# Kernel tuning notes

Measured on AMD Instinct MI355X. Metric: run time of the kernel, lower is better.

Reference implementation:

```python
import jax, jax.numpy as jnp
import numpy as np

NUM_HEADS = 16
ROPE_BASE = 10000.0


def _rope_cos_sin(T, head_dim, dtype):
    # standard rotary: angles[t, i] = t * base^(-2i/head_dim), half-split layout
    inv_freq = 1.0 / (ROPE_BASE ** (jnp.arange(0, head_dim, 2, dtype=jnp.float32) / head_dim))
    ang = jnp.arange(T, dtype=jnp.float32)[:, None] * inv_freq[None, :]  # [T, hd/2]
    cos = jnp.concatenate([jnp.cos(ang), jnp.cos(ang)], axis=-1).astype(dtype)  # [T, hd]
    sin = jnp.concatenate([jnp.sin(ang), jnp.sin(ang)], axis=-1).astype(dtype)
    return cos, sin


def _rotate_half(t):
    t1, t2 = jnp.split(t, 2, axis=-1)
    return jnp.concatenate([-t2, t1], axis=-1)


def _apply_rope(t, cos, sin):
    # t: [B, H, T, hd]; cos/sin: [T, hd]
    return t * cos[None, None] + _rotate_half(t) * sin[None, None]


def setup_inputs() -> dict:
    key = jax.random.key(0)
    B, T, C = 2, 2048, 1024
    k1, k2, k3 = jax.random.split(key, 3)
    x = jax.random.normal(k1, (B, T, C), dtype=jnp.float32)
    w_attn = jax.random.normal(k2, (C, 3 * C), dtype=jnp.float32) * (C ** -0.5)
    w_proj = jax.random.normal(k3, (C, C), dtype=jnp.float32) * (C ** -0.5)
    return {"x": x, "w_attn": w_attn, "w_proj": w_proj}


def reference(x, w_attn, w_proj):
    B, T, C = x.shape
    H = NUM_HEADS
    hd = C // H

    qkv = x @ w_attn  # [B, T, 3C]
    q, k, v = jnp.split(qkv, 3, axis=-1)
    # [B, T, C] -> [B, H, T, hd]
    q = q.reshape(B, T, H, hd).transpose(0, 2, 1, 3)
    k = k.reshape(B, T, H, hd).transpose(0, 2, 1, 3)
    v = v.reshape(B, T, H, hd).transpose(0, 2, 1, 3)

    cos, sin = _rope_cos_sin(T, hd, x.dtype)
    q = _apply_rope(q, cos, sin)
    k = _apply_rope(k, cos, sin)

    scale = 1.0 / np.sqrt(hd).astype(np.float32)
    att = jnp.einsum('bhqd,bhkd->bhqk', q, k) * scale  # [B, H, T, T]
    causal = jnp.tril(jnp.ones((T, T), dtype=bool))
    att = jnp.where(causal[None, None], att, jnp.array(-jnp.inf, dtype=att.dtype))
    att = jax.nn.softmax(att, axis=-1)
    y = jnp.einsum('bhqk,bhkd->bhqd', att, v)  # [B, H, T, hd]
    y = y.transpose(0, 2, 1, 3).reshape(B, T, C)
    return y @ w_proj
```

## Files before the change

### kernel.cpp

```cpp
#include <hip/hip_runtime.h>

typedef unsigned short u16;
typedef unsigned int u32;
typedef unsigned long long u64;
typedef __attribute__((ext_vector_type(8))) short s16x8;
typedef __attribute__((ext_vector_type(8))) __bf16 bf16x8;
typedef __attribute__((ext_vector_type(4))) float fx4;
typedef __attribute__((ext_vector_type(16))) float fx16;
typedef __attribute__((ext_vector_type(2))) u32 u32x2;
typedef __attribute__((ext_vector_type(4))) u32 u32x4;

__device__ __forceinline__ fx4 mfma_16x16x32(s16x8 a, s16x8 b, fx4 c) {
  return __builtin_amdgcn_mfma_f32_16x16x32_bf16(
      __builtin_bit_cast(bf16x8, a), __builtin_bit_cast(bf16x8, b), c, 0, 0, 0);
}
__device__ __forceinline__ fx16 mfma_32x32x16(s16x8 a, s16x8 b, fx16 c) {
  return __builtin_amdgcn_mfma_f32_32x32x16_bf16(
      __builtin_bit_cast(bf16x8, a), __builtin_bit_cast(bf16x8, b), c, 0, 0, 0);
}

__device__ __forceinline__ u16 f2bf(float f) {
  u32 u = __builtin_bit_cast(u32, f);
  u32 r = u + 0x7fffu + ((u >> 16) & 1u);
  return (u16)(r >> 16);
}
__device__ __forceinline__ float bf2f(u16 h) {
  u32 u = ((u32)h) << 16;
  return __builtin_bit_cast(float, u);
}

__device__ __forceinline__ u32 cvtpk(float lo, float hi) {
  u32 r;
  asm("v_cvt_pk_bf16_f32 %0, %1, %2" : "=v"(r) : "v"(lo), "v"(hi));
  return r;
}

__device__ __forceinline__ float max3f(float a, float b, float c) {
  float r;
  asm("v_max3_f32 %0, %1, %2, %3" : "=v"(r) : "v"(a), "v"(b), "v"(c));
  return r;
}

__device__ __forceinline__ void plswap(u32& x, u32& y) {
  typedef __attribute__((ext_vector_type(2))) unsigned int uix2;
  uix2 r = __builtin_amdgcn_permlane32_swap(x, y, false, false);
  x = r[0];
  y = r[1];
}

__device__ __forceinline__ float xhalf_max(float v) {
  u32 a = __builtin_bit_cast(u32, v), b = a;
  plswap(a, b);
  return fmaxf(__builtin_bit_cast(float, a), __builtin_bit_cast(float, b));
}
__device__ __forceinline__ float xhalf_sum(float v) {
  u32 a = __builtin_bit_cast(u32, v), b = a;
  plswap(a, b);
  return __builtin_bit_cast(float, a) + __builtin_bit_cast(float, b);
}

__device__ __forceinline__ void gload16(const void* g, void* l) {
  __builtin_amdgcn_global_load_lds(
      (const __attribute__((address_space(1))) u32*)g,
      (__attribute__((address_space(3))) u32*)l, 16, 0, 0);
}

#define B_ 2
#define T_ 2048
#define C_ 1024
#define H_ 16
#define HD_ 64
#define BH_ 32
#define M_ 4096
#define CF_ 0.18033688011112042f

__global__ __launch_bounds__(256) void prep_k(
    const float* __restrict__ x, const float* __restrict__ wa,
    const float* __restrict__ wp, u16* __restrict__ xb, u16* __restrict__ waT,
    u16* __restrict__ wpT, float* __restrict__ ct, float* __restrict__ st) {
  __shared__ u16 T_s[64 * 72];
  int b = blockIdx.x, tid = threadIdx.x;
  if (b < 2048) {
    int id = b * 256 + tid;
    const fx4* p = (const fx4*)(x + (u64)id * 8);
    fx4 v0 = p[0], v1 = p[1];
    s16x8 r;
#pragma unroll
    for (int j = 0; j < 4; ++j) {
      r[j] = (short)f2bf(v0[j]);
      r[4 + j] = (short)f2bf(v1[j]);
    }
    *((s16x8*)xb + id) = r;
  } else if (b < 3072) {
    const float* W;
    u16* WT;
    int Ncols, bx, by;
    if (b < 2816) {
      int i = b - 2048;
      W = wa; WT = waT; Ncols = 3072; bx = i % 48; by = i / 48;
    } else {
      int i = b - 2816;
      W = wp; WT = wpT; Ncols = 1024; bx = i % 16; by = i / 16;
    }
    int c0 = bx * 64, r0 = by * 64;
#pragma unroll
    for (int it = 0; it < 4; ++it) {
      int idx = it * 256 + tid;
      int r = idx >> 4, c4 = (idx & 15) * 4;
      fx4 v = *(const fx4*)(W + (u64)(r0 + r) * Ncols + c0 + c4);
#pragma unroll
      for (int j = 0; j < 4; ++j) T_s[(c4 + j) * 72 + r] = f2bf(v[j]);
    }
    __syncthreads();
#pragma unroll
    for (int it = 0; it < 2; ++it) {
      int idx = it * 256 + tid;
      int rc = idx >> 3, c8 = (idx & 7) * 8;
      s16x8 v = *(const s16x8*)(T_s + rc * 72 + c8);
      *(s16x8*)(WT + (u64)(c0 + rc) * 1024 + r0 + c8) = v;
    }
  } else {
    int id = (b - 3072) * 256 + tid;
    int t = id >> 5, i = id & 31;
    float f = exp2f(-(float)i * (13.287712379549449f / 32.0f));
    float a = (float)t * f;
    float s, c;
    sincosf(a, &s, &c);
    ct[id] = c;
    st[id] = s;
  }
}

__global__ __launch_bounds__(512, 2) void gemm1_k(
    const u16* __restrict__ A, const u16* __restrict__ B,
    u16* __restrict__ Qo, u16* __restrict__ Ko, u16* __restrict__ Vo,
    const float* __restrict__ ct, const float* __restrict__ st) {
  __shared__ u16 AsS[2][256 * 64];
  __shared__ u16 BsS[2][256 * 64];
  const int K = 1024;
  int tid = threadIdx.x, lane = tid & 63, w = tid >> 6;
  int wm = w >> 2, wn = w & 3, l15 = lane & 15, l4 = lane >> 4;
  int id = blockIdx.y * 12 + blockIdx.x;
  id = (id & 7) * 24 + (id >> 3);
  int m0 = (id / 12) * 256, n0 = (id % 12) * 256;

  const u16* asrc[4];
  const u16* bsrc[4];
  int pdst[4];
#pragma unroll
  for (int q = 0; q < 4; ++q) {
    int p = w * 256 + q * 64 + lane;
    int row = p >> 3, s = (p & 7) ^ (row & 7);
    pdst[q] = p * 16;
    asrc[q] = A + (u64)(m0 + row) * K + s * 8;
    bsrc[q] = B + (u64)(n0 + row) * K + s * 8;
  }

#define G1STAGE(BUF, KOFF)                                              \
  do {                                                                  \
    _Pragma("unroll")                                                   \
    for (int q_ = 0; q_ < 4; ++q_)                                      \
      gload16(asrc[q_] + (KOFF), (char*)AsS[BUF] + pdst[q_]);           \
    _Pragma("unroll")                                                   \
    for (int q_ = 0; q_ < 4; ++q_)                                      \
      gload16(bsrc[q_] + (KOFF), (char*)BsS[BUF] + pdst[q_]);           \
  } while (0)

  fx4 acc[8][4] = {};

  G1STAGE(0, 0);
  for (int t = 0; t < 16; ++t) {
    __builtin_amdgcn_s_barrier();
    __builtin_amdgcn_sched_barrier(0);
    if (t + 1 < 16) {
      G1STAGE((t + 1) & 1, (t + 1) * 64);
      __builtin_amdgcn_sched_barrier(0);
      asm volatile("s_waitcnt vmcnt(8)" ::: "memory");
    } else {
      asm volatile("s_waitcnt vmcnt(0)" ::: "memory");
    }
    __builtin_amdgcn_s_barrier();
    __builtin_amdgcn_sched_barrier(0);
    int buf = t & 1;
    s16x8 bf[4][2];
#pragma unroll
    for (int nj = 0; nj < 4; ++nj)
#pragma unroll
      for (int ks = 0; ks < 2; ++ks) {
        int rb = wn * 64 + nj * 16 + l15;
        int sl = ks * 4 + l4;
        bf[nj][ks] = *(const s16x8*)((const char*)BsS[buf] +
                                     (rb * 8 + (sl ^ (rb & 7))) * 16);
      }
#pragma unroll
    for (int mi = 0; mi < 8; ++mi) {
      int ra = wm * 128 + mi * 16 + l15;
      s16x8 a0 = *(const s16x8*)((const char*)AsS[buf] +
                                 (ra * 8 + (l4 ^ (ra & 7))) * 16);
      s16x8 a1 = *(const s16x8*)((const char*)AsS[buf] +
                                 (ra * 8 + ((4 + l4) ^ (ra & 7))) * 16);
      __builtin_amdgcn_s_setprio(1);
#pragma unroll
      for (int nj = 0; nj < 4; ++nj) {
        acc[mi][nj] = mfma_16x16x32(a0, bf[nj][0], acc[mi][nj]);
        acc[mi][nj] = mfma_16x16x32(a1, bf[nj][1], acc[mi][nj]);
      }
      __builtin_amdgcn_s_setprio(0);
    }
  }
#undef G1STAGE

#pragma unroll
  for (int mi = 0; mi < 8; ++mi)
#pragma unroll
    for (int r = 0; r < 4; ++r) {
      int row = m0 + wm * 128 + mi * 16 + l4 * 4 + r;
      int b2 = row >> 11, t = row & (T_ - 1);
#pragma unroll
      for (int nj = 0; nj < 2; ++nj) {
        int col = n0 + wn * 64 + nj * 16 + l15;
        int qi = col >> 10, h = (col >> 6) & 15, d = nj * 16 + l15;
        float lo = acc[mi][nj][r], hi = acc[mi][nj + 2][r];
        if (qi == 2) {
          u64 vbase =
              ((((u64)(b2 * H_ + h)) * (T_ / 8) + (t >> 3)) * HD_ + d) * 8 + (t & 7);
          Vo[vbase] = f2bf(lo);
          Vo[vbase + 32 * 8] = f2bf(hi);
        } else {
          float c = ct[t * 32 + d], s = st[t * 32 + d];
          float sc = (qi == 0) ? CF_ : 1.0f;
          u16* dst = (qi == 0) ? Qo : Ko;
          u64 base = ((((u64)(b2 * H_ + h)) * 8 + (d >> 3)) * T_ + t) * 8 + (d & 7);
          dst[base] = f2bf((lo * c - hi * s) * sc);
          dst[base + (u64)4 * T_ * 8] = f2bf((hi * c + lo * s) * sc);
        }
      }
    }
}

__global__ __launch_bounds__(256, 3) void gemm_bt_k(
    const u16* __restrict__ A, const u16* __restrict__ B, float* __restrict__ C,
    int M, int N, int K) {
  __shared__ u16 AsS[3][128 * 32];
  __shared__ u16 BsS[3][128 * 32];
  int tid = threadIdx.x, lane = tid & 63, w = tid >> 6;
  int wm = w >> 1, wn = w & 1, l15 = lane & 15, l4 = lane >> 4;
  int nwg = gridDim.x * gridDim.y;
  int id = blockIdx.y * gridDim.x + blockIdx.x;
  int qq = nwg >> 3;
  id = (id & 7) * qq + (id >> 3);
  int m0 = (id / gridDim.x) * 128, n0 = (id % gridDim.x) * 128;
  fx4 acc[4][4] = {};

  const u16* asrc[2];
  const u16* bsrc[2];
#pragma unroll
  for (int g = 0; g < 2; ++g) {
    int idx = g * 256 + tid;
    int row = idx >> 2, slot = (idx & 3) ^ (row & 3);
    asrc[g] = A + (u64)(m0 + row) * K + slot * 8;
    bsrc[g] = B + (u64)(n0 + row) * K + slot * 8;
  }

#define GSTAGE(S, KOFF)                                                      \
  do {                                                                       \
    _Pragma("unroll")                                                        \
    for (int g_ = 0; g_ < 2; ++g_) {                                         \
      gload16(asrc[g_] + (KOFF), (char*)AsS[S] + g_ * 4096 + tid * 16);      \
      gload16(bsrc[g_] + (KOFF), (char*)BsS[S] + g_ * 4096 + tid * 16);      \
    }                                                                        \
  } while (0)

#define GCOMP(S)                                                             \
  do {                                                                       \
    s16x8 a_[4], b_[4];                                                      \
    _Pragma("unroll")                                                        \
    for (int mi_ = 0; mi_ < 4; ++mi_) {                                      \
      int r_ = wm * 64 + mi_ * 16 + l15;                                     \
      a_[mi_] = *(const s16x8*)((const char*)AsS[S] + r_ * 64 +              \
                                ((l4 ^ (r_ & 3)) * 16));                     \
    }                                                                        \
    _Pragma("unroll")                                                        \
    for (int ni_ = 0; ni_ < 4; ++ni_) {                                      \
      int r_ = wn * 64 + ni_ * 16 + l15;                                     \
      b_[ni_] = *(const s16x8*)((const char*)BsS[S] + r_ * 64 +              \
                                ((l4 ^ (r_ & 3)) * 16));                     \
    }                                                                        \
    _Pragma("unroll")                                                        \
    for (int mi_ = 0; mi_ < 4; ++mi_)                                        \
      _Pragma("unroll")                                                      \
      for (int ni_ = 0; ni_ < 4; ++ni_)                                      \
        acc[mi_][ni_] = mfma_16x16x32(a_[mi_], b_[ni_], acc[mi_][ni_]);      \
  } while (0)

  int NT = K >> 5;
  GSTAGE(0, 0);
  GSTAGE(1, 32);
  int s0 = 0, s1 = 1, s2 = 2;
  for (int t = 0; t < NT; ++t) {
    __builtin_amdgcn_s_barrier();
    __builtin_amdgcn_sched_barrier(0);
    if (t + 2 < NT) GSTAGE(s2, (t + 2) * 32);
    __builtin_amdgcn_sched_barrier(0);
    if (t < NT - 2)
      asm volatile("s_waitcnt vmcnt(8)" ::: "memory");
    else if (t == NT - 2)
      asm volatile("s_waitcnt vmcnt(4)" ::: "memory");
    else
      asm volatile("s_waitcnt vmcnt(0)" ::: "memory");
    __builtin_amdgcn_s_barrier();
    __builtin_amdgcn_sched_barrier(0);
    GCOMP(s0);
    int tmp = s0;
    s0 = s1;
    s1 = s2;
    s2 = tmp;
  }
#undef GSTAGE
#undef GCOMP

#pragma unroll
  for (int mi = 0; mi < 4; ++mi)
#pragma unroll
    for (int ni = 0; ni < 4; ++ni)
#pragma unroll
      for (int r = 0; r < 4; ++r) {
        u64 row = (u64)(m0 + wm * 64 + mi * 16 + l4 * 4 + r);
        int col = n0 + wn * 64 + ni * 16 + l15;
        C[row * N + col] = acc[mi][ni][r];
      }
}

#define LOADK(KC, KVI)                                                 \
  do {                                                                 \
    _Pragma("unroll")                                                  \
    for (int ks_ = 0; ks_ < 4; ++ks_)                                  \
      KC[ks_] = *(const s16x8*)(kp[ks_] + (u64)(KVI) * 256);           \
  } while (0)

#define LOADV(VC, KVI)                                                 \
  do {                                                                 \
    const u16* vk_ = vpb + (u64)(KVI) * 2048;                          \
    VC[0] = *(const s16x8*)(vk_);                                      \
    VC[1] = *(const s16x8*)(vk_ + 256);                                \
    VC[2] = *(const s16x8*)(vk_ + 1024);                               \
    VC[3] = *(const s16x8*)(vk_ + 1280);                               \
  } while (0)

#define ATTN_STEP(KC, VC, KVI)                                                \
  do {                                                                        \
    fx16 s_ = {};                                                             \
    __builtin_amdgcn_s_setprio(1);                                            \
    _Pragma("unroll")                                                         \
    for (int ks_ = 0; ks_ < 4; ++ks_)                                         \
      s_ = mfma_32x32x16(KC[ks_], qf[ks_], s_);                               \
    __builtin_amdgcn_s_setprio(0);                                            \
    if ((KVI) == jt) {                                                        \
      _Pragma("unroll")                                                       \
      for (int r_ = 0; r_ < 16; ++r_) {                                       \
        int cr_ = (r_ & 3) + 8 * (r_ >> 2) + 4 * h;                           \
        s_[r_] = (cr_ > ql) ? -1e30f : s_[r_];                                \
      }                                                                       \
    }                                                                         \
    float u0_ = max3f(s_[0], s_[1], s_[2]);                                   \
    float u1_ = max3f(s_[3], s_[4], s_[5]);                                   \
    float u2_ = max3f(s_[6], s_[7], s_[8]);                                   \
    float u3_ = max3f(s_[9], s_[10], s_[11]);                                 \
    float u4_ = max3f(s_[12], s_[13], s_[14]);                                \
    float v0_ = max3f(u0_, u1_, s_[15]);                                      \
    float v1_ = max3f(u2_, u3_, u4_);                                         \
    float rowmax_ = xhalf_max(fmaxf(v0_, v1_));                               \
    if (!__all(rowmax_ <= m + 8.f)) {                                         \
      float mnew_ = fmaxf(m, rowmax_);                                        \
      float corr_ = exp2f(m - mnew_);                                         \
      l *= corr_;                                                             \
      oL *= corr_;                                                            \
      oH *= corr_;                                                            \
      m = mnew_;                                                              \
    }                                                                         \
    float p_[16];                                                             \
    _Pragma("unroll")                                                         \
    for (int r_ = 0; r_ < 16; ++r_) p_[r_] = exp2f(s_[r_] - m);               \
    float a0_ = (p_[0] + p_[8]) + (p_[1] + p_[9]);                            \
    float a1_ = (p_[2] + p_[10]) + (p_[3] + p_[11]);                          \
    float a2_ = (p_[4] + p_[12]) + (p_[5] + p_[13]);                          \
    float a3_ = (p_[6] + p_[14]) + (p_[7] + p_[15]);                          \
    l += xhalf_sum((a0_ + a1_) + (a2_ + a3_));                                \
    u32 x0_ = cvtpk(p_[0], p_[1]), x1_ = cvtpk(p_[2], p_[3]);                 \
    u32 y0_ = cvtpk(p_[4], p_[5]), y1_ = cvtpk(p_[6], p_[7]);                 \
    plswap(x0_, y0_);                                                         \
    plswap(x1_, y1_);                                                         \
    u32x4 f0w_ = {x0_, x1_, y0_, y1_};                                        \
    u32 x2_ = cvtpk(p_[8], p_[9]), x3_ = cvtpk(p_[10], p_[11]);               \
    u32 y2_ = cvtpk(p_[12], p_[13]), y3_ = cvtpk(p_[14], p_[15]);             \
    plswap(x2_, y2_);                                                         \
    plswap(x3_, y3_);                                                         \
    u32x4 f1w_ = {x2_, x3_, y2_, y3_};                                        \
    s16x8 pf0_ = __builtin_bit_cast(s16x8, f0w_);                             \
    s16x8 pf1_ = __builtin_bit_cast(s16x8, f1w_);                             \
    __builtin_amdgcn_s_setprio(1);                                            \
    oL = mfma_32x32x16(VC[0], pf0_, oL);                                      \
    oH = mfma_32x32x16(VC[1], pf0_, oH);                                      \
    oL = mfma_32x32x16(VC[2], pf1_, oL);                                      \
    oH = mfma_32x32x16(VC[3], pf1_, oH);                                      \
    __builtin_amdgcn_s_setprio(0);                                            \
  } while (0)

#define OSTRIDE 68

__global__ __launch_bounds__(256, 3) void attn_fwd_k(
    const u16* __restrict__ Qp, const u16* __restrict__ Kp,
    const u16* __restrict__ Vp, u16* __restrict__ Y) {
  __shared__ float Ob[4 * 32 * OSTRIDE];
  __shared__ float Ml[4 * 32 * 2];
  int tid = threadIdx.x, lane = tid & 63, w = tid >> 6;
  int ql = lane & 31, h = lane >> 5;
  int bh = blockIdx.x & 31;
  int jt = 63 - (blockIdx.x >> 5);
  int q0 = jt * 32;
  int b2 = bh >> 4, head = bh & 15;
  int n = jt + 1;
  int lo = (w * n) >> 2, hi = ((w + 1) * n) >> 2;

  s16x8 qf[4];
#pragma unroll
  for (int ks = 0; ks < 4; ++ks)
    qf[ks] = *(const s16x8*)(Qp + (((u64)bh * 8 + ks * 2 + h) * T_ + q0 + ql) * 8);

  const u16* kp[4];
#pragma unroll
  for (int ks = 0; ks < 4; ++ks)
    kp[ks] = Kp + (((u64)bh * 8 + ks * 2 + h) * T_ + ql) * 8;
  const u16* vpb = Vp + (((u64)bh * (T_ / 8) + h) * HD_ + ql) * 8;

  fx16 oL = {}, oH = {};
  float m = -1e30f, l = 0.f;

  if (lo < hi) {
    s16x8 kA[4], vA[4], kB[4], vB[4];
    LOADK(kA, lo);
    LOADV(vA, lo);
    int kv = lo;
    for (; kv + 1 < hi; kv += 2) {
      LOADK(kB, kv + 1);
      LOADV(vB, kv + 1);
      ATTN_STEP(kA, vA, kv);
      if (kv + 2 < hi) {
        LOADK(kA, kv + 2);
        LOADV(vA, kv + 2);
      }
      ATTN_STEP(kB, vB, kv + 1);
    }
    if (kv < hi) ATTN_STEP(kA, vA, kv);
  }

  {
    float* ob = Ob + (w * 32 + ql) * OSTRIDE;
#pragma unroll
    for (int g = 0; g < 4; ++g) {
      fx4 a = {oL[4 * g], oL[4 * g + 1], oL[4 * g + 2], oL[4 * g + 3]};
      *(fx4*)(ob + 8 * g + 4 * h) = a;
      fx4 b = {oH[4 * g], oH[4 * g + 1], oH[4 * g + 2], oH[4 * g + 3]};
      *(fx4*)(ob + 32 + 8 * g + 4 * h) = b;
    }
    if (h == 0) {
      Ml[(w * 32 + ql) * 2] = m;
      Ml[(w * 32 + ql) * 2 + 1] = l;
    }
  }
  __syncthreads();

  {
    int q = tid >> 3, db = tid & 7;
    float mm0 = Ml[(0 * 32 + q) * 2], ll0 = Ml[(0 * 32 + q) * 2 + 1];
    float mm1 = Ml[(1 * 32 + q) * 2], ll1 = Ml[(1 * 32 + q) * 2 + 1];
    float mm2 = Ml[(2 * 32 + q) * 2], ll2 = Ml[(2 * 32 + q) * 2 + 1];
    float mm3 = Ml[(3 * 32 + q) * 2], ll3 = Ml[(3 * 32 + q) * 2 + 1];
    float mo = fmaxf(fmaxf(mm0, mm1), fmaxf(mm2, mm3));
    float w0 = exp2f(mm0 - mo), w1 = exp2f(mm1 - mo);
    float w2 = exp2f(mm2 - mo), w3 = exp2f(mm3 - mo);
    float rl = 1.0f / (ll0 * w0 + ll1 * w1 + ll2 * w2 + ll3 * w3);
    w0 *= rl; w1 *= rl; w2 *= rl; w3 *= rl;
    const float* ob = Ob + q * OSTRIDE + db * 8;
    fx4 aa = {}, bb = {};
#pragma unroll
    for (int i = 0; i < 4; ++i) {
      float wi = (i == 0) ? w0 : (i == 1) ? w1 : (i == 2) ? w2 : w3;
      fx4 pa = *(const fx4*)(ob + i * 32 * OSTRIDE);
      fx4 pb = *(const fx4*)(ob + i * 32 * OSTRIDE + 4);
      aa += wi * pa;
      bb += wi * pb;
    }
    u32x4 ow;
    ow[0] = cvtpk(aa[0], aa[1]);
    ow[1] = cvtpk(aa[2], aa[3]);
    ow[2] = cvtpk(bb[0], bb[1]);
    ow[3] = cvtpk(bb[2], bb[3]);
    int t = q0 + q;
    *(u32x4*)(Y + ((u64)(b2 * T_ + t)) * C_ + head * HD_ + db * 8) = ow;
  }
}

extern "C" void kernel_launch(void* const* d_in, const int* in_sizes, int n_in,
                              void* d_out, int out_size, void* d_ws, size_t ws_size,
                              hipStream_t stream) {
  (void)in_sizes; (void)n_in; (void)out_size; (void)ws_size;
  const float* x = (const float*)d_in[0];
  const float* w_attn = (const float*)d_in[1];
  const float* w_proj = (const float*)d_in[2];
  float* out = (float*)d_out;

  u16* xb = (u16*)d_ws;
  u16* waT = xb + (u64)M_ * C_;
  u16* wpT = waT + (u64)3 * C_ * C_;
  u16* Qp = wpT + (u64)C_ * C_;
  u16* Kp = Qp + (u64)BH_ * T_ * HD_;
  u16* Vp = Kp + (u64)BH_ * T_ * HD_;
  float* ct = (float*)(Vp + (u64)BH_ * T_ * HD_);
  float* st = ct + T_ * 32;
  u16* yb = xb;

  prep_k<<<3328, 256, 0, stream>>>(x, w_attn, w_proj, xb, waT, wpT, ct, st);

  gemm1_k<<<dim3(12, 16), 512, 0, stream>>>(xb, waT, Qp, Kp, Vp, ct, st);

  attn_fwd_k<<<2048, 256, 0, stream>>>(Qp, Kp, Vp, yb);

  gemm_bt_k<<<dim3(8, 32), 256, 0, stream>>>(yb, wpT, out, M_, C_, C_);
}
```

Before: 119.5 us.

## Restructure QKV GEMM main loop into phased schedule interleaving loads with MFMA

Rewrites the QKV projection GEMM main loop as four compute phases per K-tile. The next tile's A and B global-to-LDS loads are issued between phases, with barriers separating them, so memory traffic overlaps the MFMA work. The LDS tiles are split into 128-row halves, and each warp reads from its own half with a simpler swizzle. The cost is more barriers per iteration and a full vmcnt(0) wait at the end of each tile, which may hurt latency hiding. The second GEMM is only renamed.

Result: faster. 114.7 us (-4.0%).

```diff
diff --git a/kernel.cpp b/kernel.cpp
--- a/kernel.cpp
+++ b/kernel.cpp
@@ -131,12 +131,12 @@
   }
 }
 
-__global__ __launch_bounds__(512, 2) void gemm1_k(
+__global__ __launch_bounds__(512, 2) void gemm1_8ph(
     const u16* __restrict__ A, const u16* __restrict__ B,
     u16* __restrict__ Qo, u16* __restrict__ Ko, u16* __restrict__ Vo,
     const float* __restrict__ ct, const float* __restrict__ st) {
-  __shared__ u16 AsS[2][256 * 64];
-  __shared__ u16 BsS[2][256 * 64];
+  __shared__ u16 As[2][2][128 * 64];
+  __shared__ u16 Bs[2][2][128 * 64];
   const int K = 1024;
   int tid = threadIdx.x, lane = tid & 63, w = tid >> 6;
   int wm = w >> 2, wn = w & 3, l15 = lane & 15, l4 = lane >> 4;
@@ -144,71 +144,112 @@
   id = (id & 7) * 24 + (id >> 3);
   int m0 = (id / 12) * 256, n0 = (id % 12) * 256;
 
-  const u16* asrc[4];
-  const u16* bsrc[4];
-  int pdst[4];
-#pragma unroll
-  for (int q = 0; q < 4; ++q) {
-    int p = w * 256 + q * 64 + lane;
+  const u16* asrc[2][2];
+  const u16* bsrc[2][2];
+  int dst16[2];
+#pragma unroll
+  for (int c = 0; c < 2; ++c) {
+    int p = c * 512 + tid;
     int row = p >> 3, s = (p & 7) ^ (row & 7);
-    pdst[q] = p * 16;
-    asrc[q] = A + (u64)(m0 + row) * K + s * 8;
-    bsrc[q] = B + (u64)(n0 + row) * K + s * 8;
-  }
-
-#define G1STAGE(BUF, KOFF)                                              \
-  do {                                                                  \
-    _Pragma("unroll")                                                   \
-    for (int q_ = 0; q_ < 4; ++q_)                                      \
-      gload16(asrc[q_] + (KOFF), (char*)AsS[BUF] + pdst[q_]);           \
-    _Pragma("unroll")                                                   \
-    for (int q_ = 0; q_ < 4; ++q_)                                      \
-      gload16(bsrc[q_] + (KOFF), (char*)BsS[BUF] + pdst[q_]);           \
-  } while (0)
+    dst16[c] = p * 16;
+#pragma unroll
+    for (int hh = 0; hh < 2; ++hh) {
+      asrc[hh][c] = A + (u64)(m0 + hh * 128 + row) * K + s * 8;
+      bsrc[hh][c] = B + (u64)(n0 + hh * 128 + row) * K + s * 8;
+    }
+  }
+
+#define STAGE_A1(BUF, KOFF)                                               \
+  do {                                                                    \
+    _Pragma("unroll")                                                     \
+    for (int hh_ = 0; hh_ < 2; ++hh_)                                     \
+      _Pragma("unroll")                                                   \
+      for (int c_ = 0; c_ < 2; ++c_)                                      \
+        gload16(asrc[hh_][c_] + (KOFF), (char*)As[BUF][hh_] + dst16[c_]); \
+  } while (0)
+#define STAGE_B1(BUF, KOFF)                                               \
+  do {                                                                    \
+    _Pragma("unroll")                                                     \
+    for (int hh_ = 0; hh_ < 2; ++hh_)                                     \
+      _Pragma("unroll")                                                   \
+      for (int c_ = 0; c_ < 2; ++c_)                                      \
+        gload16(bsrc[hh_][c_] + (KOFF), (char*)Bs[BUF][hh_] + dst16[c_]); \
+  } while (0)
+
+#define RD_A(BUF, MI, KS)                                                  \
+  (*(const s16x8*)((const char*)As[BUF][wm] +                              \
+                   ((((MI)*16 + l15) * 8 +                                 \
+                     (((KS)*4 + l4) ^ (l15 & 7))) * 16)))
+#define RD_B(BUF, NJ, KS)                                                  \
+  (*(const s16x8*)((const char*)Bs[BUF][wn >> 1] +                         \
+                   ((((wn & 1) * 64 + (NJ)*16 + l15) * 8 +                 \
+                     (((KS)*4 + l4) ^ (l15 & 7))) * 16)))
 
   fx4 acc[8][4] = {};
 
-  G1STAGE(0, 0);
-  for (int t = 0; t < 16; ++t) {
+  STAGE_A1(0, 0);
+  STAGE_B1(0, 0);
+  asm volatile("s_waitcnt vmcnt(0)" ::: "memory");
+  __builtin_amdgcn_s_barrier();
+  __builtin_amdgcn_sched_barrier(0);
+
+  for (int kt = 0; kt < 16; ++kt) {
+    int buf = kt & 1;
+    int ko = (kt + 1) * 64;
+    s16x8 a[4], bb[4];
+#pragma unroll
+    for (int i = 0; i < 4; ++i) a[i] = RD_A(buf, i, 0);
+#pragma unroll
+    for (int j = 0; j < 4; ++j) bb[j] = RD_B(buf, j, 0);
+    if (kt + 1 < 16) STAGE_A1(buf ^ 1, ko);
+    __builtin_amdgcn_s_setprio(1);
+#pragma unroll
+    for (int i = 0; i < 4; ++i)
+#pragma unroll
+      for (int j = 0; j < 4; ++j)
+        acc[i][j] = mfma_16x16x32(a[i], bb[j], acc[i][j]);
+    __builtin_amdgcn_s_setprio(0);
+    __builtin_amdgcn_s_barrier();
+#pragma unroll
+    for (int i = 0; i < 4; ++i) a[i] = RD_A(buf, 4 + i, 0);
+    if (kt + 1 < 16) STAGE_B1(buf ^ 1, ko);
+    __builtin_amdgcn_s_setprio(1);
+#pragma unroll
+    for (int i = 0; i < 4; ++i)
+#pragma unroll
+      for (int j = 0; j < 4; ++j)
+        acc[4 + i][j] = mfma_16x16x32(a[i], bb[j], acc[4 + i][j]);
+    __builtin_amdgcn_s_setprio(0);
+    __builtin_amdgcn_s_barrier();
+#pragma unroll
+    for (int i = 0; i < 4; ++i) a[i] = RD_A(buf, i, 1);
+#pragma unroll
+    for (int j = 0; j < 4; ++j) bb[j] = RD_B(buf, j, 1);
+    __builtin_amdgcn_s_setprio(1);
+#pragma unroll
+    for (int i = 0; i < 4; ++i)
+#pragma unroll
+      for (int j = 0; j < 4; ++j)
+        acc[i][j] = mfma_16x16x32(a[i], bb[j], acc[i][j]);
+    __builtin_amdgcn_s_setprio(0);
+    __builtin_amdgcn_s_barrier();
+#pragma unroll
+    for (int i = 0; i < 4; ++i) a[i] = RD_A(buf, 4 + i, 1);
+    __builtin_amdgcn_s_setprio(1);
+#pragma unroll
+    for (int i = 0; i < 4; ++i)
+#pragma unroll
+      for (int j = 0; j < 4; ++j)
+        acc[4 + i][j] = mfma_16x16x32(a[i], bb[j], acc[4 + i][j]);
+    __builtin_amdgcn_s_setprio(0);
+    asm volatile("s_waitcnt vmcnt(0)" ::: "memory");
     __builtin_amdgcn_s_barrier();
     __builtin_amdgcn_sched_barrier(0);
-    if (t + 1 < 16) {
-      G1STAGE((t + 1) & 1, (t + 1) * 64);
-      __builtin_amdgcn_sched_barrier(0);
-      asm volatile("s_waitcnt vmcnt(8)" ::: "memory");
-    } else {
-      asm volatile("s_waitcnt vmcnt(0)" ::: "memory");
-    }
-    __builtin_amdgcn_s_barrier();
-    __builtin_amdgcn_sched_barrier(0);
-    int buf = t & 1;
-    s16x8 bf[4][2];
-#pragma unroll
-    for (int nj = 0; nj < 4; ++nj)
-#pragma unroll
-      for (int ks = 0; ks < 2; ++ks) {
-        int rb = wn * 64 + nj * 16 + l15;
-        int sl = ks * 4 + l4;
-        bf[nj][ks] = *(const s16x8*)((const char*)BsS[buf] +
-                                     (rb * 8 + (sl ^ (rb & 7))) * 16);
-      }
-#pragma unroll
-    for (int mi = 0; mi < 8; ++mi) {
-      int ra = wm * 128 + mi * 16 + l15;
-      s16x8 a0 = *(const s16x8*)((const char*)AsS[buf] +
-                                 (ra * 8 + (l4 ^ (ra & 7))) * 16);
-      s16x8 a1 = *(const s16x8*)((const char*)AsS[buf] +
-                                 (ra * 8 + ((4 + l4) ^ (ra & 7))) * 16);
-      __builtin_amdgcn_s_setprio(1);
-#pragma unroll
-      for (int nj = 0; nj < 4; ++nj) {
-        acc[mi][nj] = mfma_16x16x32(a0, bf[nj][0], acc[mi][nj]);
-        acc[mi][nj] = mfma_16x16x32(a1, bf[nj][1], acc[mi][nj]);
-      }
-      __builtin_amdgcn_s_setprio(0);
-    }
-  }
-#undef G1STAGE
+  }
+#undef STAGE_A1
+#undef STAGE_B1
+#undef RD_A
+#undef RD_B
 
 #pragma unroll
   for (int mi = 0; mi < 8; ++mi)
@@ -238,7 +279,7 @@
     }
 }
 
-__global__ __launch_bounds__(256, 3) void gemm_bt_k(
+__global__ __launch_bounds__(256, 3) void gemm2_k(
     const u16* __restrict__ A, const u16* __restrict__ B, float* __restrict__ C,
     int M, int N, int K) {
   __shared__ u16 AsS[3][128 * 32];
@@ -522,9 +563,9 @@
 
   prep_k<<<3328, 256, 0, stream>>>(x, w_attn, w_proj, xb, waT, wpT, ct, st);
 
-  gemm1_k<<<dim3(12, 16), 512, 0, stream>>>(xb, waT, Qp, Kp, Vp, ct, st);
+  gemm1_8ph<<<dim3(12, 16), 512, 0, stream>>>(xb, waT, Qp, Kp, Vp, ct, st);
 
   attn_fwd_k<<<2048, 256, 0, stream>>>(Qp, Kp, Vp, yb);
 
-  gemm_bt_k<<<dim3(8, 32), 256, 0, stream>>>(yb, wpT, out, M_, C_, C_);
-}
+  gemm2_k<<<dim3(8, 32), 256, 0, stream>>>(yb, wpT, out, M_, C_, C_);
+}
```
